# Performance work log

Measured on AMD Instinct MI355X. Metric: run time of the kernel, lower is better.

## Reference

```python
import jax, jax.numpy as jnp
import numpy as np
import math

N = 50_000       # points (CSR segments)
V = 500_000      # mapped views (ragged rows)
IN_MAIN, IN_MAP, IN_MOD = 64, 16, 128
NC, NC_QK = 32, 8
EPS = 1e-12


def setup_inputs() -> dict:
    key = jax.random.key(0)
    ks = jax.random.split(key, 18)
    def rn(k, shape, fan_in=None):
        s = (1.0 / math.sqrt(fan_in)) if fan_in else 1.0
        return jax.random.normal(k, shape, jnp.float32) * s
    x_main = rn(ks[0], (N, IN_MAIN))
    x_mod = rn(ks[1], (V, IN_MOD))
    x_map = rn(ks[2], (V, IN_MAP))
    # CSR pointers: monotone, csr[0]=0, csr[-1]=V (full row coverage)
    inner = jnp.sort(jax.random.randint(ks[3], (N - 1,), 0, V))
    csr_idx = jnp.concatenate([jnp.zeros(1, jnp.int32), inner.astype(jnp.int32),
                               jnp.full((1,), V, jnp.int32)])
    return {
        "x_main": x_main, "x_mod": x_mod, "x_map": x_map, "csr_idx": csr_idx,
        # E_main: MLP([in_main, nc, nc], bias=False)
        "W_main1": rn(ks[4], (IN_MAIN, NC), IN_MAIN),
        "W_main2": rn(ks[5], (NC, NC), NC),
        # E_map (DeepSetFeat): elementwise MLP + segment-max set context + fuse
        "W_map1": rn(ks[6], (IN_MAP, NC), IN_MAP),
        "W_map2": rn(ks[7], (2 * NC, NC), 2 * NC),
        # E_mod: MLP([in_mod, in_mod, in_mod], bias=False)
        "W_mod1": rn(ks[8], (IN_MOD, IN_MOD), IN_MOD),
        "W_mod2": rn(ks[9], (IN_MOD, IN_MOD), IN_MOD),
        # Q, K linear heads (nc_inner -> nc_qk * num_groups), with bias
        "WQ": rn(ks[10], (NC, NC_QK), NC), "bQ": jnp.zeros((NC_QK,), jnp.float32),
        "WK": rn(ks[11], (NC, NC_QK), NC), "bK": jnp.zeros((NC_QK,), jnp.float32),
        # Gating(num_groups=1): weight init ones, bias init zeros
        "g_w": jnp.ones((1, 1), jnp.float32), "g_b": jnp.zeros((1, 1), jnp.float32),
    }


def reference(x_main, x_mod, x_map, csr_idx,
              W_main1, W_main2, W_map1, W_map2, W_mod1, W_mod2,
              WQ, bQ, WK, bK, g_w, g_b):
    counts = csr_idx[1:] - csr_idx[:-1]                     # [N]
    dense_idx = jnp.repeat(jnp.arange(N, dtype=jnp.int32), counts,
                           total_repeat_length=V)           # [V]
    nonempty = counts > 0                                   # [N]

    # --- encoders ---
    h_main = jax.nn.relu(x_main @ W_main1) @ W_main2        # [N, NC]
    h = jax.nn.relu(x_map @ W_map1)                         # [V, NC]
    set_ctx = jax.ops.segment_max(h, dense_idx, num_segments=N)
    set_ctx = jnp.where(nonempty[:, None], set_ctx, 0.0)    # empty segs -> 0
    h_map = jax.nn.relu(jnp.concatenate([h, set_ctx[dense_idx]], axis=1) @ W_map2)  # [V, NC]
    h_mod = jax.nn.relu(x_mod @ W_mod1) @ W_mod2            # [V, IN_MOD]

    # --- Q/K compatibilities (num_groups=1) ---
    keys = h_map @ WK + bK                                  # [V, NC_QK]
    queries = (h_main @ WQ + bQ)[dense_idx]                 # [V, NC_QK]
    comp = jnp.sum(keys * queries, axis=1) / jnp.sqrt(jnp.float32(NC_QK))  # [V]

    # --- segment_softmax_csr ---
    seg_max = jax.ops.segment_max(comp, dense_idx, num_segments=N)
    seg_max = jnp.where(nonempty, seg_max, 0.0)
    cexp = jnp.exp(comp - seg_max[dense_idx])               # [V]
    seg_sum = jax.ops.segment_sum(cexp, dense_idx, num_segments=N) + EPS
    att = cexp / seg_sum[dense_idx]                         # [V]

    # --- attention-weighted pooling ---
    x_pool = jax.ops.segment_sum(h_mod * att[:, None], dense_idx, num_segments=N)  # [N, IN_MOD]

    # --- gating on per-segment max compatibility ---
    gate_in = jnp.where(nonempty, seg_max, 0.0)[:, None]    # [N, 1]
    gate = jnp.tanh(jax.nn.relu(g_w * gate_in + g_b))       # [N, 1]
    x_pool = x_pool * gate

    x_seen = nonempty
    return x_pool, x_seen
```

## Files before the change

kernel.cpp:

```cpp
#include <hip/hip_runtime.h>
#include <math.h>

#define N_PTS 50000
#define V_VIEWS 500000
#define IN_MAIN 64
#define IN_MAP 16
#define IN_MOD 128
#define NC 32
#define NC_QK 8
#define SEG_EPS 1e-12f

typedef short bf16x8 __attribute__((ext_vector_type(8)));
typedef float f32x4 __attribute__((ext_vector_type(4)));

static __device__ __forceinline__ short f2bf(float x) {
    union { float f; unsigned u; } v; v.f = x;
    unsigned r = v.u + 0x7fffu + ((v.u >> 16) & 1u);
    return (short)(r >> 16);
}


__global__ __launch_bounds__(256) void k0_setup(const int* __restrict__ csr,
                                                const float* __restrict__ Wmod1,
                                                const float* __restrict__ Wmod2,
                                                const float* __restrict__ Wm1,
                                                const float* __restrict__ Wm2,
                                                int* __restrict__ didx,
                                                float* __restrict__ pooled,
                                                float* __restrict__ ctxw,
                                                short* __restrict__ Wf,
                                                short* __restrict__ W1f,
                                                short* __restrict__ W2af,
                                                short* __restrict__ W2f) {
    int t = blockIdx.x * blockDim.x + threadIdx.x;
    int total = gridDim.x * blockDim.x;
    if (t < N_PTS) {
        int a = csr[t], b = csr[t + 1];
        for (int v = a; v < b; ++v) didx[v] = t;
    }
    for (int i = t; i < N_PTS * IN_MOD; i += total) pooled[i] = 0.f;
    for (int i = t; i < N_PTS * NC; i += total) ctxw[i] = 0.f;
    for (int i = t; i < IN_MOD * IN_MOD; i += total) {
        int e = i & 7, l = (i >> 3) & 63, j = (i >> 9) & 7, kk = i >> 12;
        int k = kk * 32 + ((l >> 4) << 3) + e;
        int ch = (j << 4) + (l & 15);
        Wf[i] = f2bf(Wmod1[k * IN_MOD + ch]);
        W2f[i] = f2bf(Wmod2[k * IN_MOD + ch]);
    }
    for (int i = t; i < 1024; i += total) {
        int e = i & 7, l = (i >> 3) & 63, j = i >> 9;
        int k = ((l >> 4) << 3) + e;
        int ch = (j << 4) + (l & 15);
        W1f[i] = (k < IN_MAP) ? f2bf(Wm1[k * NC + ch]) : (short)0;
        W2af[i] = f2bf(Wm2[k * NC + ch]);
    }
}

__global__ __launch_bounds__(256) void kA_main_q(
    const float* __restrict__ x_main, const float* __restrict__ W1,
    const float* __restrict__ W2, const float* __restrict__ WQ,
    const float* __restrict__ bQ, const float* __restrict__ WK,
    const float* __restrict__ bK,
    float* __restrict__ wq, float* __restrict__ qb) {
    __shared__ float W1l[IN_MAIN * NC];
    __shared__ float W2l[NC * NC];
    __shared__ float WQl[NC * NC_QK];
    __shared__ float WKl[NC * NC_QK];
    __shared__ float bQl[NC_QK];
    __shared__ float bKl[NC_QK];
    __shared__ float h1buf[8][NC];
    __shared__ float h2buf[8][NC];
    __shared__ float qbuf[8][NC_QK];
    int tid = threadIdx.x;
    for (int i = tid; i < IN_MAIN * NC; i += 256) W1l[i] = W1[i];
    for (int i = tid; i < NC * NC; i += 256) W2l[i] = W2[i];
    for (int i = tid; i < NC * NC_QK; i += 256) WQl[i] = WQ[i];
    for (int i = tid; i < NC * NC_QK; i += 256) WKl[i] = WK[i];
    if (tid < NC_QK) { bQl[tid] = bQ[tid]; bKl[tid] = bK[tid]; }
    __syncthreads();
    int g = tid >> 5, c = tid & 31;
    int p = blockIdx.x * 8 + g;
    float h1 = 0.f;
    if (p < N_PTS) {
        const float* xr = x_main + (size_t)p * IN_MAIN;
        for (int k = 0; k < IN_MAIN; ++k) h1 += xr[k] * W1l[k * NC + c];
        h1 = fmaxf(h1, 0.f);
    }
    h1buf[g][c] = h1;
    __syncthreads();
    float h2 = 0.f;
    for (int j = 0; j < NC; ++j) h2 += h1buf[g][j] * W2l[j * NC + c];
    h2buf[g][c] = h2;
    __syncthreads();
    if (c < NC_QK) {
        float acc = bQl[c];
        for (int j = 0; j < NC; ++j) acc += h2buf[g][j] * WQl[j * NC_QK + c];
        qbuf[g][c] = acc;
    }
    __syncthreads();
    if (p < N_PTS) {
        float w = 0.f;
        for (int j = 0; j < NC_QK; ++j) w += WKl[c * NC_QK + j] * qbuf[g][j];
        wq[(size_t)p * NC + c] = w;
        if (c == 0) {
            float b = 0.f;
            for (int j = 0; j < NC_QK; ++j) b += bKl[j] * qbuf[g][j];
            qb[p] = b;
        }
    }
}

__global__ __launch_bounds__(256) void kH_ctx(
    const float* __restrict__ x_map, const int* __restrict__ didx,
    const short* __restrict__ W1f, int* __restrict__ ctxbits,
    short* __restrict__ hbuf) {
    __shared__ float hl[4][16 * 36];
    int tid = threadIdx.x;
    int w = tid >> 6, lane = tid & 63;
    int vbase = blockIdx.x * 64 + w * 16;
    if (vbase >= V_VIEWS) return;
    const bf16x8* pW1 = (const bf16x8*)W1f;
    bf16x8 b1a = pW1[lane], b1b = pW1[64 + lane];

    bf16x8 a1 = (bf16x8){0, 0, 0, 0, 0, 0, 0, 0};
    if (lane < 32) {
        const float* xp = x_map + (size_t)(vbase + (lane & 15)) * IN_MAP + ((lane >> 4) << 3);
        float4 x0 = *(const float4*)xp;
        float4 x1 = *(const float4*)(xp + 4);
        a1[0] = f2bf(x0.x); a1[1] = f2bf(x0.y); a1[2] = f2bf(x0.z); a1[3] = f2bf(x0.w);
        a1[4] = f2bf(x1.x); a1[5] = f2bf(x1.y); a1[6] = f2bf(x1.z); a1[7] = f2bf(x1.w);
    }
    f32x4 d1a = (f32x4){0.f, 0.f, 0.f, 0.f}, d1b = (f32x4){0.f, 0.f, 0.f, 0.f};
    d1a = __builtin_amdgcn_mfma_f32_16x16x32_bf16(a1, b1a, d1a, 0, 0, 0);
    d1b = __builtin_amdgcn_mfma_f32_16x16x32_bf16(a1, b1b, d1b, 0, 0, 0);

    int c = lane & 15, kq = lane >> 4;
    int vr0 = kq << 2;
    float* hw = hl[w];
#pragma unroll
    for (int r = 0; r < 4; ++r) {
        hw[(vr0 + r) * 36 + c] = fmaxf(d1a[r], 0.f);
        hw[(vr0 + r) * 36 + c + 16] = fmaxf(d1b[r], 0.f);
    }
    const float* hr = hw + c * 36 + (kq << 3);
    float4 h0 = *(const float4*)hr;
    float4 h1 = *(const float4*)(hr + 4);
    bf16x8 a2;
    a2[0] = f2bf(h0.x); a2[1] = f2bf(h0.y); a2[2] = f2bf(h0.z); a2[3] = f2bf(h0.w);
    a2[4] = f2bf(h1.x); a2[5] = f2bf(h1.y); a2[6] = f2bf(h1.z); a2[7] = f2bf(h1.w);
    *(bf16x8*)(hbuf + (size_t)(vbase + c) * NC + (kq << 3)) = a2;

    int vg = vbase + vr0;
    int4 ss = *(const int4*)(didx + vg);
    const int* sp = (const int*)&ss;
    float ma = 0.f, mb = 0.f;
#pragma unroll
    for (int r = 0; r < 4; ++r) {
        ma = fmaxf(ma, fmaxf(d1a[r], 0.f));
        mb = fmaxf(mb, fmaxf(d1b[r], 0.f));
        bool runend = (r == 3) || (sp[r + 1] != sp[r]);
        if (runend) {
            atomicMax(&ctxbits[sp[r] * NC + c], __float_as_int(ma));
            atomicMax(&ctxbits[sp[r] * NC + c + 16], __float_as_int(mb));
            ma = 0.f; mb = 0.f;
        }
    }
}

__global__ __launch_bounds__(256) void kB2b_ctxw(
    const float* __restrict__ Wm2, float* __restrict__ ctxw) {
    __shared__ float W2bl[NC * NC];
    __shared__ float ctxl[8][NC];
    int tid = threadIdx.x;
    for (int i = tid; i < NC * NC; i += 256) W2bl[i] = Wm2[NC * NC + i];
    int g = tid >> 5, c = tid & 31;
    int s = blockIdx.x * 8 + g;
    float cv = (s < N_PTS) ? ctxw[(size_t)s * NC + c] : 0.f;
    ctxl[g][c] = cv;
    __syncthreads();
    if (s < N_PTS) {
        float val = 0.f;
        for (int j = 0; j < NC; ++j) val += ctxl[g][j] * W2bl[j * NC + c];
        ctxw[(size_t)s * NC + c] = val;
    }
}

__global__ __launch_bounds__(256) void kB3_comp(
    const short* __restrict__ hbuf, const int* __restrict__ didx,
    const short* __restrict__ W2af,
    const float* __restrict__ ctxW2b, const float* __restrict__ wq,
    const float* __restrict__ qb, float* __restrict__ comp) {
    int tid = threadIdx.x;
    int w = tid >> 6, lane = tid & 63;
    int vbase = blockIdx.x * 64 + w * 16;
    if (vbase >= V_VIEWS) return;
    const bf16x8* pW2 = (const bf16x8*)W2af;
    bf16x8 b2a = pW2[lane], b2b = pW2[64 + lane];
    int c = lane & 15, kq = lane >> 4;

    bf16x8 a2 = *(const bf16x8*)(hbuf + (size_t)(vbase + c) * NC + (kq << 3));
    f32x4 d2a = (f32x4){0.f, 0.f, 0.f, 0.f}, d2b = (f32x4){0.f, 0.f, 0.f, 0.f};
    d2a = __builtin_amdgcn_mfma_f32_16x16x32_bf16(a2, b2a, d2a, 0, 0, 0);
    d2b = __builtin_amdgcn_mfma_f32_16x16x32_bf16(a2, b2b, d2b, 0, 0, 0);

    int vr0 = kq << 2;
    int vg = vbase + vr0;
    int4 ss = *(const int4*)(didx + vg);
    const int* sp = (const int*)&ss;
    float part[4];
#pragma unroll
    for (int r = 0; r < 4; ++r) {
        size_t so = (size_t)sp[r] * NC;
        float m0 = fmaxf(d2a[r] + ctxW2b[so + c], 0.f);
        float m1 = fmaxf(d2b[r] + ctxW2b[so + c + 16], 0.f);
        part[r] = m0 * wq[so + c] + m1 * wq[so + c + 16];
    }
#pragma unroll
    for (int mask = 1; mask < 16; mask <<= 1) {
#pragma unroll
        for (int r = 0; r < 4; ++r) part[r] += __shfl_xor(part[r], mask);
    }
    if (c == 0) {
        const float inv_sqrt = 0.35355339059327373f;
        float4 o;
        o.x = (part[0] + qb[sp[0]]) * inv_sqrt;
        o.y = (part[1] + qb[sp[1]]) * inv_sqrt;
        o.z = (part[2] + qb[sp[2]]) * inv_sqrt;
        o.w = (part[3] + qb[sp[3]]) * inv_sqrt;
        *(float4*)(comp + vg) = o;
    }
}

__global__ __launch_bounds__(256) void kB4_att(
    const float* __restrict__ comp, const int* __restrict__ csr,
    float* __restrict__ segmax, float* __restrict__ invsum) {
    int wid = threadIdx.x >> 6, lane = threadIdx.x & 63;
    int seg = blockIdx.x * 4 + wid;
    if (seg >= N_PTS) return;
    int v0 = csr[seg], v1 = csr[seg + 1];
    if (v0 >= v1) {
        if (lane == 0) { segmax[seg] = 0.f; invsum[seg] = 0.f; }
        return;
    }
    float mx = -__builtin_inff();
    for (int v = v0 + lane; v < v1; v += 64) mx = fmaxf(mx, comp[v]);
    for (int o = 32; o > 0; o >>= 1) mx = fmaxf(mx, __shfl_xor(mx, o));
    float sm = 0.f;
    for (int v = v0 + lane; v < v1; v += 64) sm += __expf(comp[v] - mx);
    for (int o = 32; o > 0; o >>= 1) sm += __shfl_xor(sm, o);
    if (lane == 0) { segmax[seg] = mx; invsum[seg] = 1.f / (sm + SEG_EPS); }
}

#define VB 64
__global__ __launch_bounds__(256) void kC_pool(
    const float* __restrict__ x_mod, const short* __restrict__ Wf,
    const int* __restrict__ didx, const int* __restrict__ csr,
    const float* __restrict__ comp, const float* __restrict__ segmax,
    const float* __restrict__ invsum, float* __restrict__ pooled) {
    __shared__ float Yl[VB * 132];
    __shared__ float attl[VB];
    __shared__ int didxl[VB];
    int tid = threadIdx.x;
    int vbase = blockIdx.x * VB;
    if (tid < VB) {
        int v = vbase + tid;
        if (v < V_VIEWS) {
            int s = didx[v];
            didxl[tid] = s;
            attl[tid] = __expf(comp[v] - segmax[s]) * invsum[s];
        } else {
            didxl[tid] = didx[V_VIEWS - 1];
            attl[tid] = 0.f;
        }
    }
    __syncthreads();

    int w = tid >> 6, lane = tid & 63;
    int row16 = lane & 15;
    int kq = lane >> 4;
    int k0 = kq << 3;
    f32x4 acc[8];
    for (int j = 0; j < 8; ++j) acc[j] = (f32x4){0.f, 0.f, 0.f, 0.f};

    int v = vbase + w * 16 + row16;
    if (v >= V_VIEWS) v = V_VIEWS - 1;
    const float* xp = x_mod + (size_t)v * IN_MOD;

#pragma unroll
    for (int kk = 0; kk < 4; ++kk) {
        float4 x0 = *(const float4*)(xp + kk * 32 + k0);
        float4 x1 = *(const float4*)(xp + kk * 32 + k0 + 4);
        bf16x8 a;
        a[0] = f2bf(x0.x); a[1] = f2bf(x0.y); a[2] = f2bf(x0.z); a[3] = f2bf(x0.w);
        a[4] = f2bf(x1.x); a[5] = f2bf(x1.y); a[6] = f2bf(x1.z); a[7] = f2bf(x1.w);
        const bf16x8* wf = (const bf16x8*)(Wf + ((size_t)(kk * 8) * 64 + lane) * 8);
#pragma unroll
        for (int j = 0; j < 8; ++j) {
            bf16x8 b = wf[j * 64];
            acc[j] = __builtin_amdgcn_mfma_f32_16x16x32_bf16(a, b, acc[j], 0, 0, 0);
        }
    }
#pragma unroll
    for (int j = 0; j < 8; ++j) {
        int ch = j * 16 + row16;
        int rbase = w * 16 + (kq << 2);
#pragma unroll
        for (int r = 0; r < 4; ++r) {
            int rw = rbase + r;
            Yl[rw * 132 + ch] = fmaxf(acc[j][r], 0.f) * attl[rw];
        }
    }
    __syncthreads();
    {
        int halfid = tid >> 7, cc = tid & 127;
        int r0 = halfid << 5;
        int hb = vbase + r0;
        float s_acc = 0.f;
        int cur = didxl[r0];
        for (int r = r0; r < r0 + 32; ++r) {
            int s = didxl[r];
            if (s != cur) {
                if (csr[cur] >= hb && csr[cur + 1] <= hb + 32)
                    pooled[(size_t)cur * IN_MOD + cc] = s_acc;
                else
                    atomicAdd(&pooled[(size_t)cur * IN_MOD + cc], s_acc);
                s_acc = 0.f; cur = s;
            }
            s_acc += Yl[r * 132 + cc];
        }
        if (csr[cur] >= hb && csr[cur + 1] <= hb + 32)
            pooled[(size_t)cur * IN_MOD + cc] = s_acc;
        else
            atomicAdd(&pooled[(size_t)cur * IN_MOD + cc], s_acc);
    }
}

__global__ __launch_bounds__(256) void kD_final(
    const short* __restrict__ W2f,
    const float* __restrict__ segmax, const int* __restrict__ csr,
    const float* __restrict__ g_w, const float* __restrict__ g_b,
    float* __restrict__ out) {
    int tid = threadIdx.x;
    int w = tid >> 6, lane = tid & 63;
    int row16 = lane & 15;
    int kq = lane >> 4;
    int k0 = kq << 3;
    int rbase = blockIdx.x * 64 + w * 16;
    float gw = g_w[0], gb = g_b[0];

    int rr = rbase + row16;
    if (rr >= N_PTS) rr = N_PTS - 1;
    const float* xp = out + (size_t)rr * IN_MOD;

    f32x4 acc[8];
    for (int j = 0; j < 8; ++j) acc[j] = (f32x4){0.f, 0.f, 0.f, 0.f};
#pragma unroll
    for (int kk = 0; kk < 4; ++kk) {
        float4 x0 = *(const float4*)(xp + kk * 32 + k0);
        float4 x1 = *(const float4*)(xp + kk * 32 + k0 + 4);
        bf16x8 a;
        a[0] = f2bf(x0.x); a[1] = f2bf(x0.y); a[2] = f2bf(x0.z); a[3] = f2bf(x0.w);
        a[4] = f2bf(x1.x); a[5] = f2bf(x1.y); a[6] = f2bf(x1.z); a[7] = f2bf(x1.w);
        const bf16x8* wf = (const bf16x8*)(W2f + ((size_t)(kk * 8) * 64 + lane) * 8);
#pragma unroll
        for (int j = 0; j < 8; ++j) {
            bf16x8 b = wf[j * 64];
            acc[j] = __builtin_amdgcn_mfma_f32_16x16x32_bf16(a, b, acc[j], 0, 0, 0);
        }
    }
    float gate[4];
    int rowv[4];
#pragma unroll
    for (int r = 0; r < 4; ++r) {
        int ro = rbase + (kq << 2) + r;
        rowv[r] = ro;
        if (ro < N_PTS) {
            bool nz = csr[ro + 1] > csr[ro];
            float gin = nz ? segmax[ro] : 0.f;
            gate[r] = tanhf(fmaxf(gw * gin + gb, 0.f));
            if (row16 == 0) out[(size_t)N_PTS * IN_MOD + ro] = nz ? 1.f : 0.f;
        } else {
            gate[r] = 0.f;
        }
    }
#pragma unroll
    for (int j = 0; j < 8; ++j) {
        int ch = j * 16 + row16;
#pragma unroll
        for (int r = 0; r < 4; ++r) {
            if (rowv[r] < N_PTS)
                out[(size_t)rowv[r] * IN_MOD + ch] = acc[j][r] * gate[r];
        }
    }
}

extern "C" void kernel_launch(void* const* d_in, const int* in_sizes, int n_in,
                              void* d_out, int out_size, void* d_ws, size_t ws_size,
                              hipStream_t stream) {
    (void)in_sizes; (void)n_in; (void)out_size; (void)ws_size;
    const float* x_main = (const float*)d_in[0];
    const float* x_mod  = (const float*)d_in[1];
    const float* x_map  = (const float*)d_in[2];
    const int*   csr    = (const int*)d_in[3];
    const float* W_main1 = (const float*)d_in[4];
    const float* W_main2 = (const float*)d_in[5];
    const float* W_map1  = (const float*)d_in[6];
    const float* W_map2  = (const float*)d_in[7];
    const float* W_mod1  = (const float*)d_in[8];
    const float* W_mod2  = (const float*)d_in[9];
    const float* WQ = (const float*)d_in[10];
    const float* bQ = (const float*)d_in[11];
    const float* WK = (const float*)d_in[12];
    const float* bK = (const float*)d_in[13];
    const float* g_w = (const float*)d_in[14];
    const float* g_b = (const float*)d_in[15];
    float* out = (float*)d_out;

    char* ws = (char*)d_ws;
    int*   didx   = (int*)ws;
    float* wq     = (float*)(ws + 2000000);
    float* qb     = (float*)(ws + 8400000);
    float* ctxw   = (float*)(ws + 8600000);
    float* comp   = (float*)(ws + 15000000);
    float* segmax = (float*)(ws + 17000000);
    short* Wf     = (short*)(ws + 17200000);
    short* W1f    = (short*)(ws + 17240000);
    short* W2af   = (short*)(ws + 17244000);
    short* W2f    = (short*)(ws + 17248000);
    float* invsum = (float*)(ws + 17300000);
    short* hbuf   = (short*)(ws + 17500000);
    float* pooled = out;

    k0_setup<<<512, 256, 0, stream>>>(csr, W_mod1, W_mod2, W_map1, W_map2,
                                      didx, pooled, ctxw, Wf, W1f, W2af, W2f);
    kA_main_q<<<(N_PTS + 7) / 8, 256, 0, stream>>>(x_main, W_main1, W_main2, WQ, bQ,
                                                   WK, bK, wq, qb);
    kH_ctx<<<(V_VIEWS + 63) / 64, 256, 0, stream>>>(x_map, didx, W1f, (int*)ctxw, hbuf);
    kB2b_ctxw<<<(N_PTS + 7) / 8, 256, 0, stream>>>(W_map2, ctxw);
    kB3_comp<<<(V_VIEWS + 63) / 64, 256, 0, stream>>>(hbuf, didx, W2af,
                                                      ctxw, wq, qb, comp);
    kB4_att<<<(N_PTS + 3) / 4, 256, 0, stream>>>(comp, csr, segmax, invsum);
    kC_pool<<<(V_VIEWS + VB - 1) / VB, 256, 0, stream>>>(x_mod, Wf, didx, csr,
                                                         comp, segmax, invsum, pooled);
    kD_final<<<(N_PTS + 63) / 64, 256, 0, stream>>>(W2f, segmax, csr, g_w, g_b, out);
}
```

Measured before the change: 235.4 us.

## Merge main-Q and map-context kernels; double-tile kC_pool with x_mod prefetch

Merges the kA_main_q and kH_ctx kernels into one launch that picks its branch by block index. This removes a launch and lets the two independent stages overlap. kC_pool now handles 128 views per block in two 64-row halves. It loads the second half's x_mod rows into registers while the first half's MFMA and reduction run, to hide global-load latency. The cost is higher register pressure from the prefetched float4 arrays, which may lower occupancy. The fused kernel also carries the shared memory of both paths.

```diff
diff --git a/kernel.cpp b/kernel.cpp
--- a/kernel.cpp
+++ b/kernel.cpp
@@ -9,6 +9,9 @@
 #define NC 32
 #define NC_QK 8
 #define SEG_EPS 1e-12f
+
+#define KH_BLOCKS ((V_VIEWS + 63) / 64)
+#define KA_BLOCKS ((N_PTS + 7) / 8)
 
 typedef short bf16x8 __attribute__((ext_vector_type(8)));
 typedef float f32x4 __attribute__((ext_vector_type(4)));
@@ -56,12 +59,16 @@
     }
 }
 
-__global__ __launch_bounds__(256) void kA_main_q(
+__global__ __launch_bounds__(256) void kHA(
+    const float* __restrict__ x_map, const int* __restrict__ didx,
+    const short* __restrict__ W1f, int* __restrict__ ctxbits,
+    short* __restrict__ hbuf,
     const float* __restrict__ x_main, const float* __restrict__ W1,
     const float* __restrict__ W2, const float* __restrict__ WQ,
     const float* __restrict__ bQ, const float* __restrict__ WK,
     const float* __restrict__ bK,
     float* __restrict__ wq, float* __restrict__ qb) {
+    __shared__ float hl[4][16 * 36];
     __shared__ float W1l[IN_MAIN * NC];
     __shared__ float W2l[NC * NC];
     __shared__ float WQl[NC * NC_QK];
@@ -71,98 +78,95 @@
     __shared__ float h1buf[8][NC];
     __shared__ float h2buf[8][NC];
     __shared__ float qbuf[8][NC_QK];
+
     int tid = threadIdx.x;
-    for (int i = tid; i < IN_MAIN * NC; i += 256) W1l[i] = W1[i];
-    for (int i = tid; i < NC * NC; i += 256) W2l[i] = W2[i];
-    for (int i = tid; i < NC * NC_QK; i += 256) WQl[i] = WQ[i];
-    for (int i = tid; i < NC * NC_QK; i += 256) WKl[i] = WK[i];
-    if (tid < NC_QK) { bQl[tid] = bQ[tid]; bKl[tid] = bK[tid]; }
-    __syncthreads();
-    int g = tid >> 5, c = tid & 31;
-    int p = blockIdx.x * 8 + g;
-    float h1 = 0.f;
-    if (p < N_PTS) {
-        const float* xr = x_main + (size_t)p * IN_MAIN;
-        for (int k = 0; k < IN_MAIN; ++k) h1 += xr[k] * W1l[k * NC + c];
-        h1 = fmaxf(h1, 0.f);
-    }
-    h1buf[g][c] = h1;
-    __syncthreads();
-    float h2 = 0.f;
-    for (int j = 0; j < NC; ++j) h2 += h1buf[g][j] * W2l[j * NC + c];
-    h2buf[g][c] = h2;
-    __syncthreads();
-    if (c < NC_QK) {
-        float acc = bQl[c];
-        for (int j = 0; j < NC; ++j) acc += h2buf[g][j] * WQl[j * NC_QK + c];
-        qbuf[g][c] = acc;
-    }
-    __syncthreads();
-    if (p < N_PTS) {
-        float w = 0.f;
-        for (int j = 0; j < NC_QK; ++j) w += WKl[c * NC_QK + j] * qbuf[g][j];
-        wq[(size_t)p * NC + c] = w;
-        if (c == 0) {
-            float b = 0.f;
-            for (int j = 0; j < NC_QK; ++j) b += bKl[j] * qbuf[g][j];
-            qb[p] = b;
-        }
-    }
-}
-
-__global__ __launch_bounds__(256) void kH_ctx(
-    const float* __restrict__ x_map, const int* __restrict__ didx,
-    const short* __restrict__ W1f, int* __restrict__ ctxbits,
-    short* __restrict__ hbuf) {
-    __shared__ float hl[4][16 * 36];
-    int tid = threadIdx.x;
-    int w = tid >> 6, lane = tid & 63;
-    int vbase = blockIdx.x * 64 + w * 16;
-    if (vbase >= V_VIEWS) return;
-    const bf16x8* pW1 = (const bf16x8*)W1f;
-    bf16x8 b1a = pW1[lane], b1b = pW1[64 + lane];
-
-    bf16x8 a1 = (bf16x8){0, 0, 0, 0, 0, 0, 0, 0};
-    if (lane < 32) {
-        const float* xp = x_map + (size_t)(vbase + (lane & 15)) * IN_MAP + ((lane >> 4) << 3);
-        float4 x0 = *(const float4*)xp;
-        float4 x1 = *(const float4*)(xp + 4);
-        a1[0] = f2bf(x0.x); a1[1] = f2bf(x0.y); a1[2] = f2bf(x0.z); a1[3] = f2bf(x0.w);
-        a1[4] = f2bf(x1.x); a1[5] = f2bf(x1.y); a1[6] = f2bf(x1.z); a1[7] = f2bf(x1.w);
-    }
-    f32x4 d1a = (f32x4){0.f, 0.f, 0.f, 0.f}, d1b = (f32x4){0.f, 0.f, 0.f, 0.f};
-    d1a = __builtin_amdgcn_mfma_f32_16x16x32_bf16(a1, b1a, d1a, 0, 0, 0);
-    d1b = __builtin_amdgcn_mfma_f32_16x16x32_bf16(a1, b1b, d1b, 0, 0, 0);
-
-    int c = lane & 15, kq = lane >> 4;
-    int vr0 = kq << 2;
-    float* hw = hl[w];
-#pragma unroll
-    for (int r = 0; r < 4; ++r) {
-        hw[(vr0 + r) * 36 + c] = fmaxf(d1a[r], 0.f);
-        hw[(vr0 + r) * 36 + c + 16] = fmaxf(d1b[r], 0.f);
-    }
-    const float* hr = hw + c * 36 + (kq << 3);
-    float4 h0 = *(const float4*)hr;
-    float4 h1 = *(const float4*)(hr + 4);
-    bf16x8 a2;
-    a2[0] = f2bf(h0.x); a2[1] = f2bf(h0.y); a2[2] = f2bf(h0.z); a2[3] = f2bf(h0.w);
-    a2[4] = f2bf(h1.x); a2[5] = f2bf(h1.y); a2[6] = f2bf(h1.z); a2[7] = f2bf(h1.w);
-    *(bf16x8*)(hbuf + (size_t)(vbase + c) * NC + (kq << 3)) = a2;
-
-    int vg = vbase + vr0;
-    int4 ss = *(const int4*)(didx + vg);
-    const int* sp = (const int*)&ss;
-    float ma = 0.f, mb = 0.f;
-#pragma unroll
-    for (int r = 0; r < 4; ++r) {
-        ma = fmaxf(ma, fmaxf(d1a[r], 0.f));
-        mb = fmaxf(mb, fmaxf(d1b[r], 0.f));
-        bool runend = (r == 3) || (sp[r + 1] != sp[r]);
-        if (runend) {
-            atomicMax(&ctxbits[sp[r] * NC + c], __float_as_int(ma));
-            atomicMax(&ctxbits[sp[r] * NC + c + 16], __float_as_int(mb));
-            ma = 0.f; mb = 0.f;
+    if (blockIdx.x < KH_BLOCKS) {
+        int w = tid >> 6, lane = tid & 63;
+        int vbase = blockIdx.x * 64 + w * 16;
+        if (vbase >= V_VIEWS) return;
+        const bf16x8* pW1 = (const bf16x8*)W1f;
+        bf16x8 b1a = pW1[lane], b1b = pW1[64 + lane];
+
+        bf16x8 a1 = (bf16x8){0, 0, 0, 0, 0, 0, 0, 0};
+        if (lane < 32) {
+            const float* xp = x_map + (size_t)(vbase + (lane & 15)) * IN_MAP + ((lane >> 4) << 3);
+            float4 x0 = *(const float4*)xp;
+            float4 x1 = *(const float4*)(xp + 4);
+            a1[0] = f2bf(x0.x); a1[1] = f2bf(x0.y); a1[2] = f2bf(x0.z); a1[3] = f2bf(x0.w);
+            a1[4] = f2bf(x1.x); a1[5] = f2bf(x1.y); a1[6] = f2bf(x1.z); a1[7] = f2bf(x1.w);
+        }
+        f32x4 d1a = (f32x4){0.f, 0.f, 0.f, 0.f}, d1b = (f32x4){0.f, 0.f, 0.f, 0.f};
+        d1a = __builtin_amdgcn_mfma_f32_16x16x32_bf16(a1, b1a, d1a, 0, 0, 0);
+        d1b = __builtin_amdgcn_mfma_f32_16x16x32_bf16(a1, b1b, d1b, 0, 0, 0);
+
+        int c = lane & 15, kq = lane >> 4;
+        int vr0 = kq << 2;
+        float* hw = hl[w];
+#pragma unroll
+        for (int r = 0; r < 4; ++r) {
+            hw[(vr0 + r) * 36 + c] = fmaxf(d1a[r], 0.f);
+            hw[(vr0 + r) * 36 + c + 16] = fmaxf(d1b[r], 0.f);
+        }
+        const float* hr = hw + c * 36 + (kq << 3);
+        float4 h0 = *(const float4*)hr;
+        float4 h1 = *(const float4*)(hr + 4);
+        bf16x8 a2;
+        a2[0] = f2bf(h0.x); a2[1] = f2bf(h0.y); a2[2] = f2bf(h0.z); a2[3] = f2bf(h0.w);
+        a2[4] = f2bf(h1.x); a2[5] = f2bf(h1.y); a2[6] = f2bf(h1.z); a2[7] = f2bf(h1.w);
+        *(bf16x8*)(hbuf + (size_t)(vbase + c) * NC + (kq << 3)) = a2;
+
+        int vg = vbase + vr0;
+        int4 ss = *(const int4*)(didx + vg);
+        const int* sp = (const int*)&ss;
+        float ma = 0.f, mb = 0.f;
+#pragma unroll
+        for (int r = 0; r < 4; ++r) {
+            ma = fmaxf(ma, fmaxf(d1a[r], 0.f));
+            mb = fmaxf(mb, fmaxf(d1b[r], 0.f));
+            bool runend = (r == 3) || (sp[r + 1] != sp[r]);
+            if (runend) {
+                atomicMax(&ctxbits[sp[r] * NC + c], __float_as_int(ma));
+                atomicMax(&ctxbits[sp[r] * NC + c + 16], __float_as_int(mb));
+                ma = 0.f; mb = 0.f;
+            }
+        }
+    } else {
+        int bid = blockIdx.x - KH_BLOCKS;
+        for (int i = tid; i < IN_MAIN * NC; i += 256) W1l[i] = W1[i];
+        for (int i = tid; i < NC * NC; i += 256) W2l[i] = W2[i];
+        for (int i = tid; i < NC * NC_QK; i += 256) WQl[i] = WQ[i];
+        for (int i = tid; i < NC * NC_QK; i += 256) WKl[i] = WK[i];
+        if (tid < NC_QK) { bQl[tid] = bQ[tid]; bKl[tid] = bK[tid]; }
+        __syncthreads();
+        int g = tid >> 5, c = tid & 31;
+        int p = bid * 8 + g;
+        float h1 = 0.f;
+        if (p < N_PTS) {
+            const float* xr = x_main + (size_t)p * IN_MAIN;
+            for (int k = 0; k < IN_MAIN; ++k) h1 += xr[k] * W1l[k * NC + c];
+            h1 = fmaxf(h1, 0.f);
+        }
+        h1buf[g][c] = h1;
+        __syncthreads();
+        float h2 = 0.f;
+        for (int j = 0; j < NC; ++j) h2 += h1buf[g][j] * W2l[j * NC + c];
+        h2buf[g][c] = h2;
+        __syncthreads();
+        if (c < NC_QK) {
+            float acc = bQl[c];
+            for (int j = 0; j < NC; ++j) acc += h2buf[g][j] * WQl[j * NC_QK + c];
+            qbuf[g][c] = acc;
+        }
+        __syncthreads();
+        if (p < N_PTS) {
+            float w = 0.f;
+            for (int j = 0; j < NC_QK; ++j) w += WKl[c * NC_QK + j] * qbuf[g][j];
+            wq[(size_t)p * NC + c] = w;
+            if (c == 0) {
+                float b = 0.f;
+                for (int j = 0; j < NC_QK; ++j) b += bKl[j] * qbuf[g][j];
+                qb[p] = b;
+            }
         }
     }
 }
@@ -251,18 +255,18 @@
     if (lane == 0) { segmax[seg] = mx; invsum[seg] = 1.f / (sm + SEG_EPS); }
 }
 
-#define VB 64
+#define VB2 128
 __global__ __launch_bounds__(256) void kC_pool(
     const float* __restrict__ x_mod, const short* __restrict__ Wf,
     const int* __restrict__ didx, const int* __restrict__ csr,
     const float* __restrict__ comp, const float* __restrict__ segmax,
     const float* __restrict__ invsum, float* __restrict__ pooled) {
-    __shared__ float Yl[VB * 132];
-    __shared__ float attl[VB];
-    __shared__ int didxl[VB];
+    __shared__ float Yl[64 * 132];
+    __shared__ float attl[VB2];
+    __shared__ int didxl[VB2];
     int tid = threadIdx.x;
-    int vbase = blockIdx.x * VB;
-    if (tid < VB) {
+    int vbase = blockIdx.x * VB2;
+    if (tid < VB2) {
         int v = vbase + tid;
         if (v < V_VIEWS) {
             int s = didx[v];
@@ -279,17 +283,21 @@
     int row16 = lane & 15;
     int kq = lane >> 4;
     int k0 = kq << 3;
+
+    int v0 = vbase + w * 16 + row16;
+    if (v0 >= V_VIEWS) v0 = V_VIEWS - 1;
+    const float* xp0 = x_mod + (size_t)v0 * IN_MOD;
+    float4 xa[8];
+#pragma unroll
+    for (int kk = 0; kk < 4; ++kk) {
+        xa[kk * 2] = *(const float4*)(xp0 + kk * 32 + k0);
+        xa[kk * 2 + 1] = *(const float4*)(xp0 + kk * 32 + k0 + 4);
+    }
     f32x4 acc[8];
     for (int j = 0; j < 8; ++j) acc[j] = (f32x4){0.f, 0.f, 0.f, 0.f};
-
-    int v = vbase + w * 16 + row16;
-    if (v >= V_VIEWS) v = V_VIEWS - 1;
-    const float* xp = x_mod + (size_t)v * IN_MOD;
-
 #pragma unroll
     for (int kk = 0; kk < 4; ++kk) {
-        float4 x0 = *(const float4*)(xp + kk * 32 + k0);
-        float4 x1 = *(const float4*)(xp + kk * 32 + k0 + 4);
+        float4 x0 = xa[kk * 2], x1 = xa[kk * 2 + 1];
         bf16x8 a;
         a[0] = f2bf(x0.x); a[1] = f2bf(x0.y); a[2] = f2bf(x0.z); a[3] = f2bf(x0.w);
         a[4] = f2bf(x1.x); a[5] = f2bf(x1.y); a[6] = f2bf(x1.z); a[7] = f2bf(x1.w);
@@ -299,6 +307,15 @@
             bf16x8 b = wf[j * 64];
             acc[j] = __builtin_amdgcn_mfma_f32_16x16x32_bf16(a, b, acc[j], 0, 0, 0);
         }
+    }
+    int v1 = vbase + 64 + w * 16 + row16;
+    if (v1 >= V_VIEWS) v1 = V_VIEWS - 1;
+    const float* xp1 = x_mod + (size_t)v1 * IN_MOD;
+    float4 xb[8];
+#pragma unroll
+    for (int kk = 0; kk < 4; ++kk) {
+        xb[kk * 2] = *(const float4*)(xp1 + kk * 32 + k0);
+        xb[kk * 2 + 1] = *(const float4*)(xp1 + kk * 32 + k0 + 4);
     }
 #pragma unroll
     for (int j = 0; j < 8; ++j) {
@@ -319,6 +336,54 @@
         int cur = didxl[r0];
         for (int r = r0; r < r0 + 32; ++r) {
             int s = didxl[r];
+            if (s != cur) {
+                if (csr[cur] >= hb && csr[cur + 1] <= hb + 32)
+                    pooled[(size_t)cur * IN_MOD + cc] = s_acc;
+                else
+                    atomicAdd(&pooled[(size_t)cur * IN_MOD + cc], s_acc);
+                s_acc = 0.f; cur = s;
+            }
+            s_acc += Yl[r * 132 + cc];
+        }
+        if (csr[cur] >= hb && csr[cur + 1] <= hb + 32)
+            pooled[(size_t)cur * IN_MOD + cc] = s_acc;
+        else
+            atomicAdd(&pooled[(size_t)cur * IN_MOD + cc], s_acc);
+    }
+    __syncthreads();
+    for (int j = 0; j < 8; ++j) acc[j] = (f32x4){0.f, 0.f, 0.f, 0.f};
+#pragma unroll
+    for (int kk = 0; kk < 4; ++kk) {
+        float4 x0 = xb[kk * 2], x1 = xb[kk * 2 + 1];
+        bf16x8 a;
+        a[0] = f2bf(x0.x); a[1] = f2bf(x0.y); a[2] = f2bf(x0.z); a[3] = f2bf(x0.w);
+        a[4] = f2bf(x1.x); a[5] = f2bf(x1.y); a[6] = f2bf(x1.z); a[7] = f2bf(x1.w);
+        const bf16x8* wf = (const bf16x8*)(Wf + ((size_t)(kk * 8) * 64 + lane) * 8);
+#pragma unroll
+        for (int j = 0; j < 8; ++j) {
+            bf16x8 b = wf[j * 64];
+            acc[j] = __builtin_amdgcn_mfma_f32_16x16x32_bf16(a, b, acc[j], 0, 0, 0);
+        }
+    }
+#pragma unroll
+    for (int j = 0; j < 8; ++j) {
+        int ch = j * 16 + row16;
+        int rbase = w * 16 + (kq << 2);
+#pragma unroll
+        for (int r = 0; r < 4; ++r) {
+            int rw = rbase + r;
+            Yl[rw * 132 + ch] = fmaxf(acc[j][r], 0.f) * attl[64 + rw];
+        }
+    }
+    __syncthreads();
+    {
+        int halfid = tid >> 7, cc = tid & 127;
+        int r0 = halfid << 5;
+        int hb = vbase + 64 + r0;
+        float s_acc = 0.f;
+        int cur = didxl[64 + r0];
+        for (int r = r0; r < r0 + 32; ++r) {
+            int s = didxl[64 + r];
             if (s != cur) {
                 if (csr[cur] >= hb && csr[cur + 1] <= hb + 32)
                     pooled[(size_t)cur * IN_MOD + cc] = s_acc;
@@ -433,14 +498,14 @@
 
     k0_setup<<<512, 256, 0, stream>>>(csr, W_mod1, W_mod2, W_map1, W_map2,
                                       didx, pooled, ctxw, Wf, W1f, W2af, W2f);
-    kA_main_q<<<(N_PTS + 7) / 8, 256, 0, stream>>>(x_main, W_main1, W_main2, WQ, bQ,
+    kHA<<<KH_BLOCKS + KA_BLOCKS, 256, 0, stream>>>(x_map, didx, W1f, (int*)ctxw, hbuf,
+                                                   x_main, W_main1, W_main2, WQ, bQ,
                                                    WK, bK, wq, qb);
-    kH_ctx<<<(V_VIEWS + 63) / 64, 256, 0, stream>>>(x_map, didx, W1f, (int*)ctxw, hbuf);
     kB2b_ctxw<<<(N_PTS + 7) / 8, 256, 0, stream>>>(W_map2, ctxw);
     kB3_comp<<<(V_VIEWS + 63) / 64, 256, 0, stream>>>(hbuf, didx, W2af,
                                                       ctxw, wq, qb, comp);
     kB4_att<<<(N_PTS + 3) / 4, 256, 0, stream>>>(comp, csr, segmax, invsum);
-    kC_pool<<<(V_VIEWS + VB - 1) / VB, 256, 0, stream>>>(x_mod, Wf, didx, csr,
-                                                         comp, segmax, invsum, pooled);
+    kC_pool<<<(V_VIEWS + VB2 - 1) / VB2, 256, 0, stream>>>(x_mod, Wf, didx, csr,
+                                                           comp, segmax, invsum, pooled);
     kD_final<<<(N_PTS + 63) / 64, 256, 0, stream>>>(W2f, segmax, csr, g_w, g_b, out);
 }
```

New measurement: 276.2 us. +17.4%, slower.

## Merge main-query and map-context kernels into one launch; bf16 pool staging

Applied to the files above, without the earlier changes.

Merges the independent x_main query-projection kernel and the x_map context kernel into one launch that splits blocks by index, removing one launch and letting the two workloads run concurrently. In the pooling kernel, the attention-weighted activations are staged in LDS as bf16 instead of fp32, roughly halving shared memory use. CSR bounds for each row are preloaded into shared memory so the segment-scan loop no longer reads them from global memory, and that loop is unrolled in chunks of eight. The merged kernel allocates the union of both kernels' shared memory, which may lower occupancy, and the bf16 staging adds rounding error to the pooled sums.

```diff
diff --git a/kernel.cpp b/kernel.cpp
--- a/kernel.cpp
+++ b/kernel.cpp
@@ -10,6 +10,9 @@
 #define NC_QK 8
 #define SEG_EPS 1e-12f
 
+#define KH_BLOCKS ((V_VIEWS + 63) / 64)
+#define KA_BLOCKS ((N_PTS + 7) / 8)
+
 typedef short bf16x8 __attribute__((ext_vector_type(8)));
 typedef float f32x4 __attribute__((ext_vector_type(4)));
 
@@ -17,6 +20,9 @@
     union { float f; unsigned u; } v; v.f = x;
     unsigned r = v.u + 0x7fffu + ((v.u >> 16) & 1u);
     return (short)(r >> 16);
+}
+static __device__ __forceinline__ float bf2f(unsigned short b) {
+    union { unsigned u; float f; } v; v.u = ((unsigned)b) << 16; return v.f;
 }
 
 
@@ -56,12 +62,16 @@
     }
 }
 
-__global__ __launch_bounds__(256) void kA_main_q(
+__global__ __launch_bounds__(256) void kHA(
+    const float* __restrict__ x_map, const int* __restrict__ didx,
+    const short* __restrict__ W1f, int* __restrict__ ctxbits,
+    short* __restrict__ hbuf,
     const float* __restrict__ x_main, const float* __restrict__ W1,
     const float* __restrict__ W2, const float* __restrict__ WQ,
     const float* __restrict__ bQ, const float* __restrict__ WK,
     const float* __restrict__ bK,
     float* __restrict__ wq, float* __restrict__ qb) {
+    __shared__ float hl[4][16 * 36];
     __shared__ float W1l[IN_MAIN * NC];
     __shared__ float W2l[NC * NC];
     __shared__ float WQl[NC * NC_QK];
@@ -71,98 +81,95 @@
     __shared__ float h1buf[8][NC];
     __shared__ float h2buf[8][NC];
     __shared__ float qbuf[8][NC_QK];
+
     int tid = threadIdx.x;
-    for (int i = tid; i < IN_MAIN * NC; i += 256) W1l[i] = W1[i];
-    for (int i = tid; i < NC * NC; i += 256) W2l[i] = W2[i];
-    for (int i = tid; i < NC * NC_QK; i += 256) WQl[i] = WQ[i];
-    for (int i = tid; i < NC * NC_QK; i += 256) WKl[i] = WK[i];
-    if (tid < NC_QK) { bQl[tid] = bQ[tid]; bKl[tid] = bK[tid]; }
-    __syncthreads();
-    int g = tid >> 5, c = tid & 31;
-    int p = blockIdx.x * 8 + g;
-    float h1 = 0.f;
-    if (p < N_PTS) {
-        const float* xr = x_main + (size_t)p * IN_MAIN;
-        for (int k = 0; k < IN_MAIN; ++k) h1 += xr[k] * W1l[k * NC + c];
-        h1 = fmaxf(h1, 0.f);
-    }
-    h1buf[g][c] = h1;
-    __syncthreads();
-    float h2 = 0.f;
-    for (int j = 0; j < NC; ++j) h2 += h1buf[g][j] * W2l[j * NC + c];
-    h2buf[g][c] = h2;
-    __syncthreads();
-    if (c < NC_QK) {
-        float acc = bQl[c];
-        for (int j = 0; j < NC; ++j) acc += h2buf[g][j] * WQl[j * NC_QK + c];
-        qbuf[g][c] = acc;
-    }
-    __syncthreads();
-    if (p < N_PTS) {
-        float w = 0.f;
-        for (int j = 0; j < NC_QK; ++j) w += WKl[c * NC_QK + j] * qbuf[g][j];
-        wq[(size_t)p * NC + c] = w;
-        if (c == 0) {
-            float b = 0.f;
-            for (int j = 0; j < NC_QK; ++j) b += bKl[j] * qbuf[g][j];
-            qb[p] = b;
-        }
-    }
-}
-
-__global__ __launch_bounds__(256) void kH_ctx(
-    const float* __restrict__ x_map, const int* __restrict__ didx,
-    const short* __restrict__ W1f, int* __restrict__ ctxbits,
-    short* __restrict__ hbuf) {
-    __shared__ float hl[4][16 * 36];
-    int tid = threadIdx.x;
-    int w = tid >> 6, lane = tid & 63;
-    int vbase = blockIdx.x * 64 + w * 16;
-    if (vbase >= V_VIEWS) return;
-    const bf16x8* pW1 = (const bf16x8*)W1f;
-    bf16x8 b1a = pW1[lane], b1b = pW1[64 + lane];
-
-    bf16x8 a1 = (bf16x8){0, 0, 0, 0, 0, 0, 0, 0};
-    if (lane < 32) {
-        const float* xp = x_map + (size_t)(vbase + (lane & 15)) * IN_MAP + ((lane >> 4) << 3);
-        float4 x0 = *(const float4*)xp;
-        float4 x1 = *(const float4*)(xp + 4);
-        a1[0] = f2bf(x0.x); a1[1] = f2bf(x0.y); a1[2] = f2bf(x0.z); a1[3] = f2bf(x0.w);
-        a1[4] = f2bf(x1.x); a1[5] = f2bf(x1.y); a1[6] = f2bf(x1.z); a1[7] = f2bf(x1.w);
-    }
-    f32x4 d1a = (f32x4){0.f, 0.f, 0.f, 0.f}, d1b = (f32x4){0.f, 0.f, 0.f, 0.f};
-    d1a = __builtin_amdgcn_mfma_f32_16x16x32_bf16(a1, b1a, d1a, 0, 0, 0);
-    d1b = __builtin_amdgcn_mfma_f32_16x16x32_bf16(a1, b1b, d1b, 0, 0, 0);
-
-    int c = lane & 15, kq = lane >> 4;
-    int vr0 = kq << 2;
-    float* hw = hl[w];
-#pragma unroll
-    for (int r = 0; r < 4; ++r) {
-        hw[(vr0 + r) * 36 + c] = fmaxf(d1a[r], 0.f);
-        hw[(vr0 + r) * 36 + c + 16] = fmaxf(d1b[r], 0.f);
-    }
-    const float* hr = hw + c * 36 + (kq << 3);
-    float4 h0 = *(const float4*)hr;
-    float4 h1 = *(const float4*)(hr + 4);
-    bf16x8 a2;
-    a2[0] = f2bf(h0.x); a2[1] = f2bf(h0.y); a2[2] = f2bf(h0.z); a2[3] = f2bf(h0.w);
-    a2[4] = f2bf(h1.x); a2[5] = f2bf(h1.y); a2[6] = f2bf(h1.z); a2[7] = f2bf(h1.w);
-    *(bf16x8*)(hbuf + (size_t)(vbase + c) * NC + (kq << 3)) = a2;
-
-    int vg = vbase + vr0;
-    int4 ss = *(const int4*)(didx + vg);
-    const int* sp = (const int*)&ss;
-    float ma = 0.f, mb = 0.f;
-#pragma unroll
-    for (int r = 0; r < 4; ++r) {
-        ma = fmaxf(ma, fmaxf(d1a[r], 0.f));
-        mb = fmaxf(mb, fmaxf(d1b[r], 0.f));
-        bool runend = (r == 3) || (sp[r + 1] != sp[r]);
-        if (runend) {
-            atomicMax(&ctxbits[sp[r] * NC + c], __float_as_int(ma));
-            atomicMax(&ctxbits[sp[r] * NC + c + 16], __float_as_int(mb));
-            ma = 0.f; mb = 0.f;
+    if (blockIdx.x < KH_BLOCKS) {
+        int w = tid >> 6, lane = tid & 63;
+        int vbase = blockIdx.x * 64 + w * 16;
+        if (vbase >= V_VIEWS) return;
+        const bf16x8* pW1 = (const bf16x8*)W1f;
+        bf16x8 b1a = pW1[lane], b1b = pW1[64 + lane];
+
+        bf16x8 a1 = (bf16x8){0, 0, 0, 0, 0, 0, 0, 0};
+        if (lane < 32) {
+            const float* xp = x_map + (size_t)(vbase + (lane & 15)) * IN_MAP + ((lane >> 4) << 3);
+            float4 x0 = *(const float4*)xp;
+            float4 x1 = *(const float4*)(xp + 4);
+            a1[0] = f2bf(x0.x); a1[1] = f2bf(x0.y); a1[2] = f2bf(x0.z); a1[3] = f2bf(x0.w);
+            a1[4] = f2bf(x1.x); a1[5] = f2bf(x1.y); a1[6] = f2bf(x1.z); a1[7] = f2bf(x1.w);
+        }
+        f32x4 d1a = (f32x4){0.f, 0.f, 0.f, 0.f}, d1b = (f32x4){0.f, 0.f, 0.f, 0.f};
+        d1a = __builtin_amdgcn_mfma_f32_16x16x32_bf16(a1, b1a, d1a, 0, 0, 0);
+        d1b = __builtin_amdgcn_mfma_f32_16x16x32_bf16(a1, b1b, d1b, 0, 0, 0);
+
+        int c = lane & 15, kq = lane >> 4;
+        int vr0 = kq << 2;
+        float* hw = hl[w];
+#pragma unroll
+        for (int r = 0; r < 4; ++r) {
+            hw[(vr0 + r) * 36 + c] = fmaxf(d1a[r], 0.f);
+            hw[(vr0 + r) * 36 + c + 16] = fmaxf(d1b[r], 0.f);
+        }
+        const float* hr = hw + c * 36 + (kq << 3);
+        float4 h0 = *(const float4*)hr;
+        float4 h1 = *(const float4*)(hr + 4);
+        bf16x8 a2;
+        a2[0] = f2bf(h0.x); a2[1] = f2bf(h0.y); a2[2] = f2bf(h0.z); a2[3] = f2bf(h0.w);
+        a2[4] = f2bf(h1.x); a2[5] = f2bf(h1.y); a2[6] = f2bf(h1.z); a2[7] = f2bf(h1.w);
+        *(bf16x8*)(hbuf + (size_t)(vbase + c) * NC + (kq << 3)) = a2;
+
+        int vg = vbase + vr0;
+        int4 ss = *(const int4*)(didx + vg);
+        const int* sp = (const int*)&ss;
+        float ma = 0.f, mb = 0.f;
+#pragma unroll
+        for (int r = 0; r < 4; ++r) {
+            ma = fmaxf(ma, fmaxf(d1a[r], 0.f));
+            mb = fmaxf(mb, fmaxf(d1b[r], 0.f));
+            bool runend = (r == 3) || (sp[r + 1] != sp[r]);
+            if (runend) {
+                atomicMax(&ctxbits[sp[r] * NC + c], __float_as_int(ma));
+                atomicMax(&ctxbits[sp[r] * NC + c + 16], __float_as_int(mb));
+                ma = 0.f; mb = 0.f;
+            }
+        }
+    } else {
+        int bid = blockIdx.x - KH_BLOCKS;
+        for (int i = tid; i < IN_MAIN * NC; i += 256) W1l[i] = W1[i];
+        for (int i = tid; i < NC * NC; i += 256) W2l[i] = W2[i];
+        for (int i = tid; i < NC * NC_QK; i += 256) WQl[i] = WQ[i];
+        for (int i = tid; i < NC * NC_QK; i += 256) WKl[i] = WK[i];
+        if (tid < NC_QK) { bQl[tid] = bQ[tid]; bKl[tid] = bK[tid]; }
+        __syncthreads();
+        int g = tid >> 5, c = tid & 31;
+        int p = bid * 8 + g;
+        float h1 = 0.f;
+        if (p < N_PTS) {
+            const float* xr = x_main + (size_t)p * IN_MAIN;
+            for (int k = 0; k < IN_MAIN; ++k) h1 += xr[k] * W1l[k * NC + c];
+            h1 = fmaxf(h1, 0.f);
+        }
+        h1buf[g][c] = h1;
+        __syncthreads();
+        float h2 = 0.f;
+        for (int j = 0; j < NC; ++j) h2 += h1buf[g][j] * W2l[j * NC + c];
+        h2buf[g][c] = h2;
+        __syncthreads();
+        if (c < NC_QK) {
+            float acc = bQl[c];
+            for (int j = 0; j < NC; ++j) acc += h2buf[g][j] * WQl[j * NC_QK + c];
+            qbuf[g][c] = acc;
+        }
+        __syncthreads();
+        if (p < N_PTS) {
+            float w = 0.f;
+            for (int j = 0; j < NC_QK; ++j) w += WKl[c * NC_QK + j] * qbuf[g][j];
+            wq[(size_t)p * NC + c] = w;
+            if (c == 0) {
+                float b = 0.f;
+                for (int j = 0; j < NC_QK; ++j) b += bKl[j] * qbuf[g][j];
+                qb[p] = b;
+            }
         }
     }
 }
@@ -257,9 +264,11 @@
     const int* __restrict__ didx, const int* __restrict__ csr,
     const float* __restrict__ comp, const float* __restrict__ segmax,
     const float* __restrict__ invsum, float* __restrict__ pooled) {
-    __shared__ float Yl[VB * 132];
+    __shared__ unsigned short Ybl[VB * 136];
     __shared__ float attl[VB];
     __shared__ int didxl[VB];
+    __shared__ int csrAl[VB];
+    __shared__ int csrBl[VB];
     int tid = threadIdx.x;
     int vbase = blockIdx.x * VB;
     if (tid < VB) {
@@ -268,9 +277,14 @@
             int s = didx[v];
             didxl[tid] = s;
             attl[tid] = __expf(comp[v] - segmax[s]) * invsum[s];
+            csrAl[tid] = csr[s];
+            csrBl[tid] = csr[s + 1];
         } else {
-            didxl[tid] = didx[V_VIEWS - 1];
+            int s = didx[V_VIEWS - 1];
+            didxl[tid] = s;
             attl[tid] = 0.f;
+            csrAl[tid] = csr[s];
+            csrBl[tid] = csr[s + 1];
         }
     }
     __syncthreads();
@@ -307,7 +321,7 @@
 #pragma unroll
         for (int r = 0; r < 4; ++r) {
             int rw = rbase + r;
-            Yl[rw * 132 + ch] = fmaxf(acc[j][r], 0.f) * attl[rw];
+            Ybl[rw * 136 + ch] = (unsigned short)f2bf(fmaxf(acc[j][r], 0.f) * attl[rw]);
         }
     }
     __syncthreads();
@@ -317,18 +331,26 @@
         int hb = vbase + r0;
         float s_acc = 0.f;
         int cur = didxl[r0];
-        for (int r = r0; r < r0 + 32; ++r) {
-            int s = didxl[r];
-            if (s != cur) {
-                if (csr[cur] >= hb && csr[cur + 1] <= hb + 32)
-                    pooled[(size_t)cur * IN_MOD + cc] = s_acc;
-                else
-                    atomicAdd(&pooled[(size_t)cur * IN_MOD + cc], s_acc);
-                s_acc = 0.f; cur = s;
+        int curA = csrAl[r0], curB = csrBl[r0];
+        for (int rc = 0; rc < 32; rc += 8) {
+            float yv[8];
+#pragma unroll
+            for (int u = 0; u < 8; ++u) yv[u] = bf2f(Ybl[(r0 + rc + u) * 136 + cc]);
+#pragma unroll
+            for (int u = 0; u < 8; ++u) {
+                int r = r0 + rc + u;
+                int s = didxl[r];
+                if (s != cur) {
+                    if (curA >= hb && curB <= hb + 32)
+                        pooled[(size_t)cur * IN_MOD + cc] = s_acc;
+                    else
+                        atomicAdd(&pooled[(size_t)cur * IN_MOD + cc], s_acc);
+                    s_acc = 0.f; cur = s; curA = csrAl[r]; curB = csrBl[r];
+                }
+                s_acc += yv[u];
             }
-            s_acc += Yl[r * 132 + cc];
-        }
-        if (csr[cur] >= hb && csr[cur + 1] <= hb + 32)
+        }
+        if (curA >= hb && curB <= hb + 32)
             pooled[(size_t)cur * IN_MOD + cc] = s_acc;
         else
             atomicAdd(&pooled[(size_t)cur * IN_MOD + cc], s_acc);
@@ -433,9 +455,9 @@
 
     k0_setup<<<512, 256, 0, stream>>>(csr, W_mod1, W_mod2, W_map1, W_map2,
                                       didx, pooled, ctxw, Wf, W1f, W2af, W2f);
-    kA_main_q<<<(N_PTS + 7) / 8, 256, 0, stream>>>(x_main, W_main1, W_main2, WQ, bQ,
+    kHA<<<KH_BLOCKS + KA_BLOCKS, 256, 0, stream>>>(x_map, didx, W1f, (int*)ctxw, hbuf,
+                                                   x_main, W_main1, W_main2, WQ, bQ,
                                                    WK, bK, wq, qb);
-    kH_ctx<<<(V_VIEWS + 63) / 64, 256, 0, stream>>>(x_map, didx, W1f, (int*)ctxw, hbuf);
     kB2b_ctxw<<<(N_PTS + 7) / 8, 256, 0, stream>>>(W_map2, ctxw);
     kB3_comp<<<(V_VIEWS + 63) / 64, 256, 0, stream>>>(hbuf, didx, W2af,
                                                       ctxw, wq, qb, comp);
```

After: 221.6 us. -5.9%, faster.
